# Kernel optimization log

Measured on AMD Instinct MI355X. Metric: run time of the kernel, lower is better.

Reference implementation:

```python
import jax, jax.numpy as jnp
import numpy as np

B, TQ, TK, D, H = 2, 2048, 2048, 1024, 16
HD = D // H
MLP = 4 * D
EPS = 1e-5


def _ln(x, g, b):
    m = jnp.mean(x, axis=-1, keepdims=True)
    v = jnp.mean(jnp.square(x - m), axis=-1, keepdims=True)
    return (x - m) * jax.lax.rsqrt(v + EPS) * g + b


def setup_inputs() -> dict:
    key = jax.random.key(0)
    ks = jax.random.split(key, 16)
    s = 0.02
    inp = {
        "x": jax.random.normal(ks[0], (B, TQ, D), jnp.float32),
        "enc_out": jax.random.normal(ks[1], (B, TK, D), jnp.float32),
        "causal_mask": jnp.tril(jnp.ones((TQ, TQ), jnp.int32)),
        # LayerNorm params
        "ln1_g": jnp.ones((D,), jnp.float32), "ln1_b": jnp.zeros((D,), jnp.float32),
        "ln2_g": jnp.ones((D,), jnp.float32), "ln2_b": jnp.zeros((D,), jnp.float32),
        "ln3_g": jnp.ones((D,), jnp.float32), "ln3_b": jnp.zeros((D,), jnp.float32),
        # self-attn (weights stored [in, out])
        "qkv_w": jax.random.normal(ks[2], (D, 3 * D), jnp.float32) * s,
        "qkv_b": jnp.zeros((3 * D,), jnp.float32),
        "proj_w": jax.random.normal(ks[3], (D, D), jnp.float32) * s,
        "proj_b": jnp.zeros((D,), jnp.float32),
        # cross-attn
        "q_w": jax.random.normal(ks[4], (D, D), jnp.float32) * s,
        "q_b": jnp.zeros((D,), jnp.float32),
        "kv_w": jax.random.normal(ks[5], (D, 2 * D), jnp.float32) * s,
        "kv_b": jnp.zeros((2 * D,), jnp.float32),
        "co_w": jax.random.normal(ks[6], (D, D), jnp.float32) * s,
        "co_b": jnp.zeros((D,), jnp.float32),
        # MLP
        "mlp1_w": jax.random.normal(ks[7], (D, MLP), jnp.float32) * s,
        "mlp1_b": jnp.zeros((MLP,), jnp.float32),
        "mlp2_w": jax.random.normal(ks[8], (MLP, D), jnp.float32) * s,
        "mlp2_b": jnp.zeros((D,), jnp.float32),
    }
    return inp


def _self_attn(x, mask, qkv_w, qkv_b, proj_w, proj_b):
    b, t, d = x.shape
    qkv = (x @ qkv_w + qkv_b).reshape(b, t, 3, H, HD)
    q, k, v = qkv[:, :, 0], qkv[:, :, 1], qkv[:, :, 2]  # [b,t,H,HD]
    scale = HD ** (-0.5)
    attn = jnp.einsum('bqhd,bkhd->bhqk', q, k) * scale
    attn = jnp.where(mask[None, None] == 0, -jnp.inf, attn)
    attn = jax.nn.softmax(attn, axis=-1)
    out = jnp.einsum('bhqk,bkhd->bqhd', attn, v).reshape(b, t, d)
    return out @ proj_w + proj_b


def _cross_attn(q_in, kv_in, q_w, q_b, kv_w, kv_b, co_w, co_b):
    b, tq, d = q_in.shape
    tk = kv_in.shape[1]
    Q = (q_in @ q_w + q_b).reshape(b, tq, H, HD)
    KV = (kv_in @ kv_w + kv_b).reshape(b, tk, 2, H, HD)
    K, V = KV[:, :, 0], KV[:, :, 1]
    scale = HD ** (-0.5)
    attn = jnp.einsum('bqhd,bkhd->bhqk', Q, K) * scale
    attn = jax.nn.softmax(attn, axis=-1)
    out = jnp.einsum('bhqk,bkhd->bqhd', attn, V).reshape(b, tq, d)
    return out @ co_w + co_b


def reference(x, enc_out, causal_mask, ln1_g, ln1_b, ln2_g, ln2_b, ln3_g, ln3_b,
              qkv_w, qkv_b, proj_w, proj_b, q_w, q_b, kv_w, kv_b, co_w, co_b,
              mlp1_w, mlp1_b, mlp2_w, mlp2_b):
    x = x + _self_attn(_ln(x, ln1_g, ln1_b), causal_mask, qkv_w, qkv_b, proj_w, proj_b)
    x = x + _cross_attn(_ln(x, ln2_g, ln2_b), enc_out, q_w, q_b, kv_w, kv_b, co_w, co_b)
    h = _ln(x, ln3_g, ln3_b)
    h = jax.nn.gelu(h @ mlp1_w + mlp1_b, approximate=False) @ mlp2_w + mlp2_b
    return x + h
```

## Files before the change

kernel.cpp:

```cpp
#include <hip/hip_runtime.h>
#include <hip/hip_bf16.h>
#include <cstdint>
#include <cstddef>


#define DEV __device__ __forceinline__

typedef short bf16x8 __attribute__((ext_vector_type(8)));
typedef float f32x4  __attribute__((ext_vector_type(4)));

DEV unsigned short f2bf(float f) {
  unsigned int u = __builtin_bit_cast(unsigned int, f);
  u = u + 0x7FFFu + ((u >> 16) & 1u);
  return (unsigned short)(u >> 16);
}

DEV void gload_lds16(const void* g, void* lds) {
  __builtin_amdgcn_global_load_lds(
      (const __attribute__((address_space(1))) void*)g,
      (__attribute__((address_space(3))) void*)lds, 16, 0, 0);
}

__global__ __launch_bounds__(256) void k_transpose_bf16(
    const float* __restrict__ in, unsigned short* __restrict__ out, int K, int N) {
  __shared__ float tile[32][33];
  const int n0 = blockIdx.x * 32, k0 = blockIdx.y * 32;
  const int tx = threadIdx.x, ty = threadIdx.y;
#pragma unroll
  for (int i = 0; i < 32; i += 8)
    tile[ty + i][tx] = in[(size_t)(k0 + ty + i) * N + n0 + tx];
  __syncthreads();
#pragma unroll
  for (int i = 0; i < 32; i += 8)
    out[(size_t)(n0 + ty + i) * K + k0 + tx] = f2bf(tile[tx][ty + i]);
}

__global__ __launch_bounds__(256) void k_vtrans(
    const unsigned short* __restrict__ V, int ldv, int vo0,
    unsigned short* __restrict__ vt, int TK) {
  __shared__ unsigned short tile[32][33];
  const int k0 = blockIdx.x * 32;
  const int d0 = (blockIdx.y & 1) * 32;
  const int bh = blockIdx.z;
  const int b = bh >> 4, h = bh & 15;
  const int tx = threadIdx.x, ty = threadIdx.y;
  const size_t tok0 = (size_t)b * 2048;
#pragma unroll
  for (int i = 0; i < 32; i += 8)
    tile[ty + i][tx] = V[(tok0 + k0 + ty + i) * ldv + vo0 + h * 64 + d0 + tx];
  __syncthreads();
#pragma unroll
  for (int i = 0; i < 32; i += 8)
    vt[((size_t)bh * 64 + d0 + ty + i) * TK + k0 + tx] = tile[tx][ty + i];
}

__global__ __launch_bounds__(256) void k_f32_to_bf16(
    const float* __restrict__ in, unsigned short* __restrict__ out, int n4) {
  const int i = blockIdx.x * 256 + threadIdx.x;
  if (i < n4) {
    const float4 v = ((const float4*)in)[i];
    ushort4 o;
    o.x = f2bf(v.x); o.y = f2bf(v.y); o.z = f2bf(v.z); o.w = f2bf(v.w);
    ((ushort4*)out)[i] = o;
  }
}

__global__ __launch_bounds__(256) void k_ln(
    const float* __restrict__ x, const float* __restrict__ g,
    const float* __restrict__ bt, unsigned short* __restrict__ y) {
  const int row = blockIdx.x, t = threadIdx.x;
  const float4 v = ((const float4*)(x + (size_t)row * 1024))[t];
  float s1 = v.x + v.y + v.z + v.w;
  float s2 = v.x * v.x + v.y * v.y + v.z * v.z + v.w * v.w;
#pragma unroll
  for (int off = 1; off < 64; off <<= 1) {
    s1 += __shfl_xor(s1, off);
    s2 += __shfl_xor(s2, off);
  }
  __shared__ float r1[4], r2[4];
  if ((t & 63) == 0) { r1[t >> 6] = s1; r2[t >> 6] = s2; }
  __syncthreads();
  const float tot1 = r1[0] + r1[1] + r1[2] + r1[3];
  const float tot2 = r2[0] + r2[1] + r2[2] + r2[3];
  const float mean = tot1 * (1.0f / 1024.0f);
  const float var  = tot2 * (1.0f / 1024.0f) - mean * mean;
  const float rstd = rsqrtf(var + 1e-5f);
  const float4 gg = ((const float4*)g)[t];
  const float4 bb = ((const float4*)bt)[t];
  ushort4 o;
  o.x = f2bf((v.x - mean) * rstd * gg.x + bb.x);
  o.y = f2bf((v.y - mean) * rstd * gg.y + bb.y);
  o.z = f2bf((v.z - mean) * rstd * gg.z + bb.z);
  o.w = f2bf((v.w - mean) * rstd * gg.w + bb.w);
  ((ushort4*)(y + (size_t)row * 1024))[t] = o;
}

template <int EPI>
__global__ __launch_bounds__(256) void k_gemm(
    const unsigned short* __restrict__ A, const unsigned short* __restrict__ Bt,
    const float* __restrict__ bias, const float* __restrict__ resid,
    unsigned short* __restrict__ Obf, float* __restrict__ Of, int N, int K) {
  __shared__ __align__(16) unsigned short As[128 * 32];
  __shared__ __align__(16) unsigned short Bs[128 * 32];
  const int tid = threadIdx.x;
  const int wave = tid >> 6, lane = tid & 63;
  const int nwg = gridDim.x * gridDim.y;
  const int wg = blockIdx.y * gridDim.x + blockIdx.x;
  const int swz = (wg & 7) * (nwg >> 3) + (wg >> 3);
  const int bn = swz % gridDim.x, bm = swz / gridDim.x;
  const int la = lane & 15, ks = (lane >> 4) * 8;
  const int wr = wave >> 1, wc = wave & 1;
  f32x4 acc[4][4] = {};
  const int r0 = wave * 32 + (lane >> 2);
  const int kk = (lane & 3) * 8;
  const unsigned short* ga = A  + (size_t)(bm * 128 + r0) * K + kk;
  const unsigned short* gb = Bt + (size_t)(bn * 128 + r0) * K + kk;
  unsigned short* lA0 = &As[(wave * 32) * 32];
  unsigned short* lA1 = &As[(wave * 32 + 16) * 32];
  unsigned short* lB0 = &Bs[(wave * 32) * 32];
  unsigned short* lB1 = &Bs[(wave * 32 + 16) * 32];
  for (int kt = 0; kt < K; kt += 32) {
    gload_lds16(ga + kt,                  lA0);
    gload_lds16(ga + kt + (size_t)16 * K, lA1);
    gload_lds16(gb + kt,                  lB0);
    gload_lds16(gb + kt + (size_t)16 * K, lB1);
    __syncthreads();
    bf16x8 af[4], bfr[4];
#pragma unroll
    for (int m = 0; m < 4; ++m)
      af[m] = *(const bf16x8*)&As[(wr * 64 + m * 16 + la) * 32 + ks];
#pragma unroll
    for (int n = 0; n < 4; ++n)
      bfr[n] = *(const bf16x8*)&Bs[(wc * 64 + n * 16 + la) * 32 + ks];
#pragma unroll
    for (int m = 0; m < 4; ++m)
#pragma unroll
      for (int n = 0; n < 4; ++n)
        acc[m][n] = __builtin_amdgcn_mfma_f32_16x16x32_bf16(af[m], bfr[n], acc[m][n], 0, 0, 0);
    __syncthreads();
  }
#pragma unroll
  for (int m = 0; m < 4; ++m) {
    const int row = bm * 128 + wr * 64 + m * 16 + (lane >> 4) * 4;
#pragma unroll
    for (int n = 0; n < 4; ++n) {
      const int col = bn * 128 + wc * 64 + n * 16 + la;
      const float bv = bias[col];
#pragma unroll
      for (int r = 0; r < 4; ++r) {
        float v = acc[m][n][r] + bv;
        const size_t idx = (size_t)(row + r) * N + col;
        if constexpr (EPI == 0) {
          Obf[idx] = f2bf(v);
        } else if constexpr (EPI == 1) {
          Of[idx] = v + resid[idx];
        } else {
          v = 0.5f * v * (1.0f + erff(v * 0.70710678118654752f));
          Obf[idx] = f2bf(v);
        }
      }
    }
  }
}

template <bool CAUSAL>
__global__ __launch_bounds__(256) void k_attn3(
    const unsigned short* __restrict__ Qb, int ldq, int qo0,
    const unsigned short* __restrict__ Kb, int ldk, int ko0,
    const unsigned short* __restrict__ Vtg,
    unsigned short* __restrict__ O, int TK) {
  __shared__ __align__(16) unsigned short Ks[2][64 * 64];
  __shared__ __align__(16) unsigned short Vs[2][64 * 64];
  __shared__ __align__(16) unsigned short Pl[4][16 * 64];
  const int qt = (blockIdx.x + blockIdx.y) & 31;
  const int h = blockIdx.y, b = blockIdx.z;
  const int bh = b * 16 + h;
  const int tid = threadIdx.x, wave = tid >> 6, lane = tid & 63;
  const int la = lane & 15, g = lane >> 4;
  const int qoff = qo0 + h * 64, koff = ko0 + h * 64;
  const size_t tok0 = (size_t)b * 2048;
  constexpr float SCALE = 0.125f * 1.44269504088896f;

  bf16x8 qf[2];
  {
    const unsigned short* qp =
        Qb + (tok0 + qt * 64 + wave * 16 + la) * ldq + qoff + g * 8;
    qf[0] = *(const bf16x8*)qp;
    qf[1] = *(const bf16x8*)(qp + 32);
  }
  f32x4 oacc[4] = {};
  float m_r = -1e30f, l_r = 0.0f;

  const int nkt = CAUSAL ? (qt + 1) : (TK >> 6);

  const int rr = lane >> 3, cc = lane & 7;
  const int sc = (cc ^ rr) * 8;
  const unsigned short* Vrow = Vtg + (size_t)bh * 64 * TK;
  auto stage = [&](int kt, int buf) {
#pragma unroll
    for (int r = 0; r < 2; ++r) {
      const int row = wave * 8 + r * 32 + rr;
      gload_lds16(Kb + (tok0 + kt * 64 + row) * ldk + koff + sc,
                  &Ks[buf][(wave * 8 + r * 32) * 64]);
      gload_lds16(Vrow + (size_t)row * TK + kt * 64 + sc,
                  &Vs[buf][(wave * 8 + r * 32) * 64]);
    }
  };

  stage(0, 0);
  int cur = 0;
  char* pw = (char*)Pl[wave];
  const int lsw = (la & 7) << 4;

  for (int kt = 0; kt < nkt; ++kt) {
    if (kt + 1 < nkt) {
      stage(kt + 1, cur ^ 1);
      asm volatile("s_waitcnt vmcnt(4)" ::: "memory");
    } else {
      asm volatile("s_waitcnt vmcnt(0)" ::: "memory");
    }
    __builtin_amdgcn_s_barrier();

    f32x4 s[4] = {};
    __builtin_amdgcn_s_setprio(1);
#pragma unroll
    for (int kc = 0; kc < 2; ++kc)
#pragma unroll
      for (int n = 0; n < 4; ++n) {
        const int key = n * 16 + la;
        const bf16x8 kfr = *(const bf16x8*)((const char*)&Ks[cur][0] +
            key * 128 + ((kc * 64 + g * 16) ^ ((key & 7) << 4)));
        s[n] = __builtin_amdgcn_mfma_f32_16x16x32_bf16(kfr, qf[kc], s[n], 0, 0, 0);
      }
    __builtin_amdgcn_s_setprio(0);

    float xx[4][4];
#pragma unroll
    for (int n = 0; n < 4; ++n)
#pragma unroll
      for (int r = 0; r < 4; ++r) xx[n][r] = s[n][r] * SCALE;
    if (CAUSAL && kt == nkt - 1) {
      const int qloc = wave * 16 + la;
#pragma unroll
      for (int n = 0; n < 4; ++n)
#pragma unroll
        for (int r = 0; r < 4; ++r)
          if (n * 16 + g * 4 + r > qloc) xx[n][r] = -1e30f;
    }
    float t0 = fmaxf(fmaxf(xx[0][0], xx[0][1]), fmaxf(xx[0][2], xx[0][3]));
    float t1 = fmaxf(fmaxf(xx[1][0], xx[1][1]), fmaxf(xx[1][2], xx[1][3]));
    float t2 = fmaxf(fmaxf(xx[2][0], xx[2][1]), fmaxf(xx[2][2], xx[2][3]));
    float t3 = fmaxf(fmaxf(xx[3][0], xx[3][1]), fmaxf(xx[3][2], xx[3][3]));
    float tm = fmaxf(fmaxf(t0, t1), fmaxf(t2, t3));
    tm = fmaxf(tm, __shfl_xor(tm, 16, 64));
    tm = fmaxf(tm, __shfl_xor(tm, 32, 64));
    const float mn = fmaxf(m_r, tm);
    const float al = exp2f(m_r - mn);
    m_r = mn;
    float p[4][4];
#pragma unroll
    for (int n = 0; n < 4; ++n)
#pragma unroll
      for (int r = 0; r < 4; ++r) p[n][r] = exp2f(xx[n][r] - mn);
    float rs = ((p[0][0] + p[0][1]) + (p[0][2] + p[0][3]))
             + ((p[1][0] + p[1][1]) + (p[1][2] + p[1][3]))
             + ((p[2][0] + p[2][1]) + (p[2][2] + p[2][3]))
             + ((p[3][0] + p[3][1]) + (p[3][2] + p[3][3]));
    rs += __shfl_xor(rs, 16, 64);
    rs += __shfl_xor(rs, 32, 64);
    l_r = l_r * al + rs;
#pragma unroll
    for (int n4 = 0; n4 < 4; ++n4)
#pragma unroll
      for (int r = 0; r < 4; ++r) oacc[n4][r] *= al;

#pragma unroll
    for (int n = 0; n < 4; ++n)
#pragma unroll
      for (int rp = 0; rp < 2; ++rp) {
        const unsigned int w = (unsigned int)f2bf(p[n][2 * rp]) |
                               ((unsigned int)f2bf(p[n][2 * rp + 1]) << 16);
        *(unsigned int*)(pw + la * 128 + ((n * 32 + g * 8 + rp * 4) ^ lsw)) = w;
      }
    asm volatile("s_waitcnt lgkmcnt(0)" ::: "memory");
    bf16x8 pb[2];
    pb[0] = *(const bf16x8*)(pw + la * 128 + ((0 * 64 + g * 16) ^ lsw));
    pb[1] = *(const bf16x8*)(pw + la * 128 + ((1 * 64 + g * 16) ^ lsw));

    __builtin_amdgcn_s_setprio(1);
#pragma unroll
    for (int kc = 0; kc < 2; ++kc)
#pragma unroll
      for (int n4 = 0; n4 < 4; ++n4) {
        const int d = n4 * 16 + la;
        const bf16x8 vb = *(const bf16x8*)((const char*)&Vs[cur][0] +
            d * 128 + ((kc * 64 + g * 16) ^ ((d & 7) << 4)));
        oacc[n4] = __builtin_amdgcn_mfma_f32_16x16x32_bf16(vb, pb[kc], oacc[n4], 0, 0, 0);
      }
    __builtin_amdgcn_s_setprio(0);
    asm volatile("s_waitcnt lgkmcnt(0)" ::: "memory");
    __builtin_amdgcn_s_barrier();
    cur ^= 1;
  }

  const float inv = 1.0f / l_r;
#pragma unroll
  for (int n4 = 0; n4 < 4; ++n4)
#pragma unroll
    for (int rp = 0; rp < 2; ++rp) {
      const unsigned int w = (unsigned int)f2bf(oacc[n4][2 * rp] * inv) |
                             ((unsigned int)f2bf(oacc[n4][2 * rp + 1] * inv) << 16);
      *(unsigned int*)(pw + la * 128 + ((n4 * 32 + g * 8 + rp * 4) ^ lsw)) = w;
    }
  asm volatile("s_waitcnt lgkmcnt(0)" ::: "memory");
  const int q2 = lane >> 2, c4 = lane & 3;
  const size_t orow = tok0 + qt * 64 + wave * 16 + q2;
#pragma unroll
  for (int h8 = 0; h8 < 2; ++h8) {
    const bf16x8 v = *(const bf16x8*)(pw + q2 * 128 +
        ((c4 * 32 + h8 * 16) ^ ((q2 & 7) << 4)));
    *(bf16x8*)&O[orow * 1024 + h * 64 + c4 * 16 + h8 * 8] = v;
  }
}

constexpr size_t SZ_1K1K  = 1024ull * 1024 * 2;
constexpr size_t OFF_WQKV = 0;                         constexpr size_t SZ_WQKV = 3072ull * 1024 * 2;
constexpr size_t OFF_WPRJ = OFF_WQKV + SZ_WQKV;
constexpr size_t OFF_WQ   = OFF_WPRJ + SZ_1K1K;
constexpr size_t OFF_WKV  = OFF_WQ + SZ_1K1K;          constexpr size_t SZ_WKV = 2048ull * 1024 * 2;
constexpr size_t OFF_WCO  = OFF_WKV + SZ_WKV;
constexpr size_t OFF_WM1  = OFF_WCO + SZ_1K1K;         constexpr size_t SZ_WM1 = 4096ull * 1024 * 2;
constexpr size_t OFF_WM2  = OFF_WM1 + SZ_WM1;          constexpr size_t SZ_WM2 = 1024ull * 4096 * 2;
constexpr size_t OFF_ENCB = OFF_WM2 + SZ_WM2;          constexpr size_t SZ_ACT = 4096ull * 1024 * 2;
constexpr size_t OFF_XCUR = OFF_ENCB + SZ_ACT;         constexpr size_t SZ_XF  = 4096ull * 1024 * 4;
constexpr size_t OFF_LNO  = OFF_XCUR + SZ_XF;
constexpr size_t OFF_BIG  = OFF_LNO + SZ_ACT;          constexpr size_t SZ_BIG = 4096ull * 4096 * 2;
constexpr size_t OFF_ATTN = OFF_BIG + SZ_BIG;
constexpr size_t OFF_QPRJ = OFF_ATTN + SZ_ACT;
constexpr size_t WS_NEED  = OFF_QPRJ + SZ_ACT;

extern "C" void kernel_launch(void* const* d_in, const int* in_sizes, int n_in,
                              void* d_out, int out_size, void* d_ws, size_t ws_size,
                              hipStream_t stream) {
  (void)in_sizes; (void)n_in; (void)out_size;
  if (ws_size < WS_NEED) return;

  const float* x     = (const float*)d_in[0];
  const float* enc   = (const float*)d_in[1];
  const float* ln1g  = (const float*)d_in[3];
  const float* ln1b  = (const float*)d_in[4];
  const float* ln2g  = (const float*)d_in[5];
  const float* ln2b  = (const float*)d_in[6];
  const float* ln3g  = (const float*)d_in[7];
  const float* ln3b  = (const float*)d_in[8];
  const float* qkv_w = (const float*)d_in[9];
  const float* qkv_b = (const float*)d_in[10];
  const float* prj_w = (const float*)d_in[11];
  const float* prj_b = (const float*)d_in[12];
  const float* q_w   = (const float*)d_in[13];
  const float* q_b   = (const float*)d_in[14];
  const float* kv_w  = (const float*)d_in[15];
  const float* kv_b  = (const float*)d_in[16];
  const float* co_w  = (const float*)d_in[17];
  const float* co_b  = (const float*)d_in[18];
  const float* m1_w  = (const float*)d_in[19];
  const float* m1_b  = (const float*)d_in[20];
  const float* m2_w  = (const float*)d_in[21];
  const float* m2_b  = (const float*)d_in[22];
  float* out = (float*)d_out;

  char* ws = (char*)d_ws;
  unsigned short* wqkv = (unsigned short*)(ws + OFF_WQKV);
  unsigned short* wprj = (unsigned short*)(ws + OFF_WPRJ);
  unsigned short* wq   = (unsigned short*)(ws + OFF_WQ);
  unsigned short* wkv  = (unsigned short*)(ws + OFF_WKV);
  unsigned short* wco  = (unsigned short*)(ws + OFF_WCO);
  unsigned short* wm1  = (unsigned short*)(ws + OFF_WM1);
  unsigned short* wm2  = (unsigned short*)(ws + OFF_WM2);
  unsigned short* encb = (unsigned short*)(ws + OFF_ENCB);
  float*          xcur = (float*)(ws + OFF_XCUR);
  unsigned short* lno  = (unsigned short*)(ws + OFF_LNO);
  unsigned short* big  = (unsigned short*)(ws + OFF_BIG);
  unsigned short* attnb= (unsigned short*)(ws + OFF_ATTN);
  unsigned short* qprj = (unsigned short*)(ws + OFF_QPRJ);
  unsigned short* vtS  = big + (size_t)4096 * 3072;
  unsigned short* vtC  = big + (size_t)4096 * 2048;

  const dim3 tb(32, 8);
  k_transpose_bf16<<<dim3(3072/32, 1024/32), tb, 0, stream>>>(qkv_w, wqkv, 1024, 3072);
  k_transpose_bf16<<<dim3(1024/32, 1024/32), tb, 0, stream>>>(prj_w, wprj, 1024, 1024);
  k_transpose_bf16<<<dim3(1024/32, 1024/32), tb, 0, stream>>>(q_w,   wq,   1024, 1024);
  k_transpose_bf16<<<dim3(2048/32, 1024/32), tb, 0, stream>>>(kv_w,  wkv,  1024, 2048);
  k_transpose_bf16<<<dim3(1024/32, 1024/32), tb, 0, stream>>>(co_w,  wco,  1024, 1024);
  k_transpose_bf16<<<dim3(4096/32, 1024/32), tb, 0, stream>>>(m1_w,  wm1,  1024, 4096);
  k_transpose_bf16<<<dim3(1024/32, 4096/32), tb, 0, stream>>>(m2_w,  wm2,  4096, 1024);
  k_f32_to_bf16<<<4096, 256, 0, stream>>>(enc, encb, 1048576);

  k_ln<<<4096, 256, 0, stream>>>(x, ln1g, ln1b, lno);
  k_gemm<0><<<dim3(24, 32), 256, 0, stream>>>(lno, wqkv, qkv_b, nullptr, big, nullptr, 3072, 1024);
  k_vtrans<<<dim3(64, 2, 32), tb, 0, stream>>>(big, 3072, 2048, vtS, 2048);
  k_attn3<true><<<dim3(32, 16, 2), 256, 0, stream>>>(big, 3072, 0,
                                                     big, 3072, 1024,
                                                     vtS, attnb, 2048);
  k_gemm<1><<<dim3(8, 32), 256, 0, stream>>>(attnb, wprj, prj_b, x, nullptr, xcur, 1024, 1024);

  k_ln<<<4096, 256, 0, stream>>>(xcur, ln2g, ln2b, lno);
  k_gemm<0><<<dim3(8, 32), 256, 0, stream>>>(lno,  wq,  q_b,  nullptr, qprj, nullptr, 1024, 1024);
  k_gemm<0><<<dim3(16, 32), 256, 0, stream>>>(encb, wkv, kv_b, nullptr, big,  nullptr, 2048, 1024);
  k_vtrans<<<dim3(64, 2, 32), tb, 0, stream>>>(big, 2048, 1024, vtC, 2048);
  k_attn3<false><<<dim3(32, 16, 2), 256, 0, stream>>>(qprj, 1024, 0,
                                                      big,  2048, 0,
                                                      vtC, attnb, 2048);
  k_gemm<1><<<dim3(8, 32), 256, 0, stream>>>(attnb, wco, co_b, xcur, nullptr, xcur, 1024, 1024);

  k_ln<<<4096, 256, 0, stream>>>(xcur, ln3g, ln3b, lno);
  k_gemm<2><<<dim3(32, 32), 256, 0, stream>>>(lno, wm1, m1_b, nullptr, big, nullptr, 4096, 1024);
  k_gemm<1><<<dim3(8, 32), 256, 0, stream>>>(big, wm2, m2_b, xcur, nullptr, out, 1024, 4096);
}
```

Baseline: 692.9 us.

## Fold softmax scale into Q weights, add lazy rescale and packed bf16 convert

Pre-multiplies the Q projection weights and biases by the attention scale times log2(e) during weight conversion, which removes the per-element scaling multiply in the attention inner loop. The online-softmax max update and the rescaling of the accumulator are now skipped unless some row's max rises by more than 8 (a lazy rescale). The manual bf16 rounding is replaced with the hardware v_cvt_pk_bf16_f32 instruction. The trade-off is that rounding the scaled Q to bf16 changes numerics slightly, and the lazy rescale lets probabilities reach up to 2^8 before renormalisation.

```diff
diff --git a/kernel.cpp b/kernel.cpp
--- a/kernel.cpp
+++ b/kernel.cpp
@@ -9,12 +9,20 @@
 typedef short bf16x8 __attribute__((ext_vector_type(8)));
 typedef float f32x4  __attribute__((ext_vector_type(4)));
 
+#define QSCALE 0.18033688011112042f
+
 DEV unsigned short f2bf(float f) {
   unsigned int u = __builtin_bit_cast(unsigned int, f);
   u = u + 0x7FFFu + ((u >> 16) & 1u);
   return (unsigned short)(u >> 16);
 }
 
+DEV unsigned int cvt_pk_bf16(float lo, float hi) {
+  unsigned int r;
+  asm volatile("v_cvt_pk_bf16_f32 %0, %1, %2" : "=v"(r) : "v"(lo), "v"(hi));
+  return r;
+}
+
 DEV void gload_lds16(const void* g, void* lds) {
   __builtin_amdgcn_global_load_lds(
       (const __attribute__((address_space(1))) void*)g,
@@ -22,7 +30,8 @@
 }
 
 __global__ __launch_bounds__(256) void k_transpose_bf16(
-    const float* __restrict__ in, unsigned short* __restrict__ out, int K, int N) {
+    const float* __restrict__ in, unsigned short* __restrict__ out, int K, int N,
+    int s0, int s1, float sc) {
   __shared__ float tile[32][33];
   const int n0 = blockIdx.x * 32, k0 = blockIdx.y * 32;
   const int tx = threadIdx.x, ty = threadIdx.y;
@@ -31,8 +40,18 @@
     tile[ty + i][tx] = in[(size_t)(k0 + ty + i) * N + n0 + tx];
   __syncthreads();
 #pragma unroll
-  for (int i = 0; i < 32; i += 8)
-    out[(size_t)(n0 + ty + i) * K + k0 + tx] = f2bf(tile[tx][ty + i]);
+  for (int i = 0; i < 32; i += 8) {
+    const int n = n0 + ty + i;
+    float v = tile[tx][ty + i];
+    if (n >= s0 && n < s1) v *= sc;
+    out[(size_t)n * K + k0 + tx] = f2bf(v);
+  }
+}
+
+__global__ __launch_bounds__(256) void k_scale_bias(
+    const float* __restrict__ in, float* __restrict__ out, int n, int s0, int s1, float sc) {
+  const int i = blockIdx.x * 256 + threadIdx.x;
+  if (i < n) out[i] = in[i] * ((i >= s0 && i < s1) ? sc : 1.0f);
 }
 
 __global__ __launch_bounds__(256) void k_vtrans(
@@ -164,7 +183,7 @@
 }
 
 template <bool CAUSAL>
-__global__ __launch_bounds__(256) void k_attn3(
+__global__ __launch_bounds__(256) void k_attn4(
     const unsigned short* __restrict__ Qb, int ldq, int qo0,
     const unsigned short* __restrict__ Kb, int ldk, int ko0,
     const unsigned short* __restrict__ Vtg,
@@ -179,7 +198,6 @@
   const int la = lane & 15, g = lane >> 4;
   const int qoff = qo0 + h * 64, koff = ko0 + h * 64;
   const size_t tok0 = (size_t)b * 2048;
-  constexpr float SCALE = 0.125f * 1.44269504088896f;
 
   bf16x8 qf[2];
   {
@@ -234,52 +252,49 @@
       }
     __builtin_amdgcn_s_setprio(0);
 
-    float xx[4][4];
-#pragma unroll
-    for (int n = 0; n < 4; ++n)
-#pragma unroll
-      for (int r = 0; r < 4; ++r) xx[n][r] = s[n][r] * SCALE;
     if (CAUSAL && kt == nkt - 1) {
       const int qloc = wave * 16 + la;
 #pragma unroll
       for (int n = 0; n < 4; ++n)
 #pragma unroll
         for (int r = 0; r < 4; ++r)
-          if (n * 16 + g * 4 + r > qloc) xx[n][r] = -1e30f;
-    }
-    float t0 = fmaxf(fmaxf(xx[0][0], xx[0][1]), fmaxf(xx[0][2], xx[0][3]));
-    float t1 = fmaxf(fmaxf(xx[1][0], xx[1][1]), fmaxf(xx[1][2], xx[1][3]));
-    float t2 = fmaxf(fmaxf(xx[2][0], xx[2][1]), fmaxf(xx[2][2], xx[2][3]));
-    float t3 = fmaxf(fmaxf(xx[3][0], xx[3][1]), fmaxf(xx[3][2], xx[3][3]));
+          if (n * 16 + g * 4 + r > qloc) s[n][r] = -1e30f;
+    }
+    float t0 = fmaxf(fmaxf(s[0][0], s[0][1]), fmaxf(s[0][2], s[0][3]));
+    float t1 = fmaxf(fmaxf(s[1][0], s[1][1]), fmaxf(s[1][2], s[1][3]));
+    float t2 = fmaxf(fmaxf(s[2][0], s[2][1]), fmaxf(s[2][2], s[2][3]));
+    float t3 = fmaxf(fmaxf(s[3][0], s[3][1]), fmaxf(s[3][2], s[3][3]));
     float tm = fmaxf(fmaxf(t0, t1), fmaxf(t2, t3));
     tm = fmaxf(tm, __shfl_xor(tm, 16, 64));
     tm = fmaxf(tm, __shfl_xor(tm, 32, 64));
-    const float mn = fmaxf(m_r, tm);
-    const float al = exp2f(m_r - mn);
-    m_r = mn;
+    if (!__all(tm <= m_r + 8.0f)) {
+      const float mn = fmaxf(m_r, tm);
+      const float al = exp2f(m_r - mn);
+      m_r = mn;
+      l_r *= al;
+#pragma unroll
+      for (int n4 = 0; n4 < 4; ++n4)
+#pragma unroll
+        for (int r = 0; r < 4; ++r) oacc[n4][r] *= al;
+    }
     float p[4][4];
 #pragma unroll
     for (int n = 0; n < 4; ++n)
 #pragma unroll
-      for (int r = 0; r < 4; ++r) p[n][r] = exp2f(xx[n][r] - mn);
+      for (int r = 0; r < 4; ++r) p[n][r] = exp2f(s[n][r] - m_r);
     float rs = ((p[0][0] + p[0][1]) + (p[0][2] + p[0][3]))
              + ((p[1][0] + p[1][1]) + (p[1][2] + p[1][3]))
              + ((p[2][0] + p[2][1]) + (p[2][2] + p[2][3]))
              + ((p[3][0] + p[3][1]) + (p[3][2] + p[3][3]));
     rs += __shfl_xor(rs, 16, 64);
     rs += __shfl_xor(rs, 32, 64);
-    l_r = l_r * al + rs;
-#pragma unroll
-    for (int n4 = 0; n4 < 4; ++n4)
-#pragma unroll
-      for (int r = 0; r < 4; ++r) oacc[n4][r] *= al;
+    l_r += rs;
 
 #pragma unroll
     for (int n = 0; n < 4; ++n)
 #pragma unroll
       for (int rp = 0; rp < 2; ++rp) {
-        const unsigned int w = (unsigned int)f2bf(p[n][2 * rp]) |
-                               ((unsigned int)f2bf(p[n][2 * rp + 1]) << 16);
+        const unsigned int w = cvt_pk_bf16(p[n][2 * rp], p[n][2 * rp + 1]);
         *(unsigned int*)(pw + la * 128 + ((n * 32 + g * 8 + rp * 4) ^ lsw)) = w;
       }
     asm volatile("s_waitcnt lgkmcnt(0)" ::: "memory");
@@ -308,8 +323,7 @@
   for (int n4 = 0; n4 < 4; ++n4)
 #pragma unroll
     for (int rp = 0; rp < 2; ++rp) {
-      const unsigned int w = (unsigned int)f2bf(oacc[n4][2 * rp] * inv) |
-                             ((unsigned int)f2bf(oacc[n4][2 * rp + 1] * inv) << 16);
+      const unsigned int w = cvt_pk_bf16(oacc[n4][2 * rp] * inv, oacc[n4][2 * rp + 1] * inv);
       *(unsigned int*)(pw + la * 128 + ((n4 * 32 + g * 8 + rp * 4) ^ lsw)) = w;
     }
   asm volatile("s_waitcnt lgkmcnt(0)" ::: "memory");
@@ -337,7 +351,9 @@
 constexpr size_t OFF_BIG  = OFF_LNO + SZ_ACT;          constexpr size_t SZ_BIG = 4096ull * 4096 * 2;
 constexpr size_t OFF_ATTN = OFF_BIG + SZ_BIG;
 constexpr size_t OFF_QPRJ = OFF_ATTN + SZ_ACT;
-constexpr size_t WS_NEED  = OFF_QPRJ + SZ_ACT;
+constexpr size_t OFF_BQKV = OFF_QPRJ + SZ_ACT;
+constexpr size_t OFF_BQ   = OFF_BQKV + 3072 * 4;
+constexpr size_t WS_NEED  = OFF_BQ + 1024 * 4;
 
 extern "C" void kernel_launch(void* const* d_in, const int* in_sizes, int n_in,
                               void* d_out, int out_size, void* d_ws, size_t ws_size,
@@ -383,32 +399,36 @@
   unsigned short* big  = (unsigned short*)(ws + OFF_BIG);
   unsigned short* attnb= (unsigned short*)(ws + OFF_ATTN);
   unsigned short* qprj = (unsigned short*)(ws + OFF_QPRJ);
+  float*          bqkv = (float*)(ws + OFF_BQKV);
+  float*          bq   = (float*)(ws + OFF_BQ);
   unsigned short* vtS  = big + (size_t)4096 * 3072;
   unsigned short* vtC  = big + (size_t)4096 * 2048;
 
   const dim3 tb(32, 8);
-  k_transpose_bf16<<<dim3(3072/32, 1024/32), tb, 0, stream>>>(qkv_w, wqkv, 1024, 3072);
-  k_transpose_bf16<<<dim3(1024/32, 1024/32), tb, 0, stream>>>(prj_w, wprj, 1024, 1024);
-  k_transpose_bf16<<<dim3(1024/32, 1024/32), tb, 0, stream>>>(q_w,   wq,   1024, 1024);
-  k_transpose_bf16<<<dim3(2048/32, 1024/32), tb, 0, stream>>>(kv_w,  wkv,  1024, 2048);
-  k_transpose_bf16<<<dim3(1024/32, 1024/32), tb, 0, stream>>>(co_w,  wco,  1024, 1024);
-  k_transpose_bf16<<<dim3(4096/32, 1024/32), tb, 0, stream>>>(m1_w,  wm1,  1024, 4096);
-  k_transpose_bf16<<<dim3(1024/32, 4096/32), tb, 0, stream>>>(m2_w,  wm2,  4096, 1024);
+  k_transpose_bf16<<<dim3(3072/32, 1024/32), tb, 0, stream>>>(qkv_w, wqkv, 1024, 3072, 0, 1024, QSCALE);
+  k_transpose_bf16<<<dim3(1024/32, 1024/32), tb, 0, stream>>>(prj_w, wprj, 1024, 1024, 0, 0, 1.0f);
+  k_transpose_bf16<<<dim3(1024/32, 1024/32), tb, 0, stream>>>(q_w,   wq,   1024, 1024, 0, 1024, QSCALE);
+  k_transpose_bf16<<<dim3(2048/32, 1024/32), tb, 0, stream>>>(kv_w,  wkv,  1024, 2048, 0, 0, 1.0f);
+  k_transpose_bf16<<<dim3(1024/32, 1024/32), tb, 0, stream>>>(co_w,  wco,  1024, 1024, 0, 0, 1.0f);
+  k_transpose_bf16<<<dim3(4096/32, 1024/32), tb, 0, stream>>>(m1_w,  wm1,  1024, 4096, 0, 0, 1.0f);
+  k_transpose_bf16<<<dim3(1024/32, 4096/32), tb, 0, stream>>>(m2_w,  wm2,  4096, 1024, 0, 0, 1.0f);
+  k_scale_bias<<<12, 256, 0, stream>>>(qkv_b, bqkv, 3072, 0, 1024, QSCALE);
+  k_scale_bias<<<4, 256, 0, stream>>>(q_b, bq, 1024, 0, 1024, QSCALE);
   k_f32_to_bf16<<<4096, 256, 0, stream>>>(enc, encb, 1048576);
 
   k_ln<<<4096, 256, 0, stream>>>(x, ln1g, ln1b, lno);
-  k_gemm<0><<<dim3(24, 32), 256, 0, stream>>>(lno, wqkv, qkv_b, nullptr, big, nullptr, 3072, 1024);
+  k_gemm<0><<<dim3(24, 32), 256, 0, stream>>>(lno, wqkv, bqkv, nullptr, big, nullptr, 3072, 1024);
   k_vtrans<<<dim3(64, 2, 32), tb, 0, stream>>>(big, 3072, 2048, vtS, 2048);
-  k_attn3<true><<<dim3(32, 16, 2), 256, 0, stream>>>(big, 3072, 0,
+  k_attn4<true><<<dim3(32, 16, 2), 256, 0, stream>>>(big, 3072, 0,
                                                      big, 3072, 1024,
                                                      vtS, attnb, 2048);
   k_gemm<1><<<dim3(8, 32), 256, 0, stream>>>(attnb, wprj, prj_b, x, nullptr, xcur, 1024, 1024);
 
   k_ln<<<4096, 256, 0, stream>>>(xcur, ln2g, ln2b, lno);
-  k_gemm<0><<<dim3(8, 32), 256, 0, stream>>>(lno,  wq,  q_b,  nullptr, qprj, nullptr, 1024, 1024);
+  k_gemm<0><<<dim3(8, 32), 256, 0, stream>>>(lno,  wq,  bq,   nullptr, qprj, nullptr, 1024, 1024);
   k_gemm<0><<<dim3(16, 32), 256, 0, stream>>>(encb, wkv, kv_b, nullptr, big,  nullptr, 2048, 1024);
   k_vtrans<<<dim3(64, 2, 32), tb, 0, stream>>>(big, 2048, 1024, vtC, 2048);
-  k_attn3<false><<<dim3(32, 16, 2), 256, 0, stream>>>(qprj, 1024, 0,
+  k_attn4<false><<<dim3(32, 16, 2), 256, 0, stream>>>(qprj, 1024, 0,
                                                       big,  2048, 0,
                                                       vtC, attnb, 2048);
   k_gemm<1><<<dim3(8, 32), 256, 0, stream>>>(attnb, wco, co_b, xcur, nullptr, xcur, 1024, 1024);
```

New measurement: 676.3 us. 1.02x faster.
